# Performance work log

Measured on AMD Instinct MI355X. Metric: run time of the kernel, lower is better.

The kernel has to match this reference:

```python
import jax, jax.numpy as jnp
import numpy as np

B, C, H, W, K = 16, 64, 192, 192, 3

def setup_inputs() -> dict:
    key = jax.random.key(0)
    k1, k2, k3, k4 = jax.random.split(key, 4)
    x = jax.random.normal(k1, (B, C, H, W), dtype=jnp.float32)
    DoT = jax.random.uniform(k2, (B,), dtype=jnp.float32)
    W0 = jax.random.normal(k3, (C, C, K, K), dtype=jnp.float32) * 0.05
    W1 = jax.random.normal(k4, (C, C, K, K), dtype=jnp.float32) * 0.05
    return {"x": x, "DoT": DoT, "W0": W0, "W1": W1}

def reference(x, DoT, W0, W1):
    # Per-sample blended kernels: [B, C_o, C_i, K, K]
    d = DoT[:, None, None, None, None]
    kernel = (1.0 - d) * W0[None] + d * W1[None]

    def conv_one(xi, ki):
        # xi: [C_i, H, W], ki: [C_o, C_i, K, K]
        out = jax.lax.conv_general_dilated(
            xi[None], ki,
            window_strides=(1, 1),
            padding=((1, 1), (1, 1)),
            dimension_numbers=("NCHW", "OIHW", "NCHW"),
        )
        return out[0]

    y = jax.vmap(conv_one)(x, kernel)  # [B, C_o, H, W]
    return y
```

## Files before the change

kernel.cpp:

```cpp
#include <hip/hip_runtime.h>
#include <hip/hip_bf16.h>
#include <stdint.h>

#define NB 16
#define NC 64
#define NH 192
#define NW 192
#define NKDIM 576

typedef __bf16 bf16x8 __attribute__((ext_vector_type(8)));
typedef __bf16 bf16x4 __attribute__((ext_vector_type(4)));
typedef float  f32x4  __attribute__((ext_vector_type(4)));

static __device__ __forceinline__ __bf16 f2bf(float f) { return (__bf16)f; }

__global__ __launch_bounds__(256)
void blend_kernel(const float* __restrict__ W0, const float* __restrict__ W1,
                  const float* __restrict__ DoT, __bf16* __restrict__ A) {
    int idx = blockIdx.x * 256 + threadIdx.x;
    int k   = idx % NKDIM;
    int co  = (idx / NKDIM) % NC;
    int b   = idx / (NKDIM * NC);
    int tap = k >> 6;
    int ci  = k & 63;
    float d  = DoT[b];
    int wi   = (co * NC + ci) * 9 + tap;
    float v  = (1.0f - d) * W0[wi] + d * W1[wi];
    A[idx] = f2bf(v);
}

__global__ __launch_bounds__(256)
void nhwc_cvt_kernel(const float* __restrict__ x, __bf16* __restrict__ xt) {
    __shared__ float tile[64 * 68];

    const int b  = blockIdx.z;
    const int h  = blockIdx.y;
    const int wt = blockIdx.x * 64;
    const int t  = threadIdx.x;

    {
        const int ci = t & 63;
        const int wq = t >> 6;
        const float* src = x + ((size_t)(b * NC + ci) * NH + h) * NW + wt;
        #pragma unroll
        for (int w4l = 0; w4l < 4; ++w4l) {
            const int w4 = wq * 4 + w4l;
            f32x4 v = *(const f32x4*)(src + w4 * 4);
            #pragma unroll
            for (int j = 0; j < 4; ++j)
                tile[(w4 * 4 + j) * 68 + ci] = v[j];
        }
    }
    __syncthreads();

    __bf16* dst = xt + ((size_t)(b * NH + h) * NW + wt) * NC;
    #pragma unroll
    for (int it = 0; it < 2; ++it) {
        const int c   = it * 256 + t;
        const int w   = c >> 3;
        const int cig = c & 7;
        f32x4 v0 = *(const f32x4*)&tile[w * 68 + cig * 8];
        f32x4 v1 = *(const f32x4*)&tile[w * 68 + cig * 8 + 4];
        bf16x8 pk = { f2bf(v0[0]), f2bf(v0[1]), f2bf(v0[2]), f2bf(v0[3]),
                      f2bf(v1[0]), f2bf(v1[1]), f2bf(v1[2]), f2bf(v1[3]) };
        *(bf16x8*)(dst + (size_t)w * NC + cig * 8) = pk;
    }
}

__global__ __launch_bounds__(512, 4)
void conv_nhwc_kernel(const __bf16* __restrict__ xt, const __bf16* __restrict__ A,
                      float* __restrict__ out) {
    __shared__ __bf16 xs[4 * 66 * 8 * 8];

    const int b  = blockIdx.z;
    const int h0 = blockIdx.y * 2;
    const int w0 = blockIdx.x * 64;

    const int tid  = threadIdx.x;
    const int lane = tid & 63;
    const int wave = tid >> 6;

    {
        #pragma unroll
        for (int it = 0; it < 4; ++it) {
            const int c   = it * 512 + tid;
            const int r   = c / 528;
            const int rem = c - r * 528;
            const int w   = rem >> 3;
            const int g   = rem & 7;
            const int gr  = h0 - 1 + r;
            const int gw  = w0 - 1 + w;
            const bool ok = (gr >= 0) && (gr < NH) && (gw >= 0) && (gw < NW);
            bf16x8 v = {};
            if (ok)
                v = *(const bf16x8*)(xt + ((size_t)(b * NH + gr) * NW + gw) * NC + g * 8);
            *(bf16x8*)&xs[(((r * 66 + w) * 8) + (g ^ (w & 7))) * 8] = v;
        }
        if (tid < 64) {
            const int c   = 2048 + tid;
            const int r   = 3;
            const int rem = c - 3 * 528;
            const int w   = rem >> 3;
            const int g   = rem & 7;
            const int gr  = h0 + 2;
            const int gw  = w0 - 1 + w;
            const bool ok = (gr < NH) && (gw < NW);
            bf16x8 v = {};
            if (ok)
                v = *(const bf16x8*)(xt + ((size_t)(b * NH + gr) * NW + gw) * NC + g * 8);
            *(bf16x8*)&xs[(((r * 66 + w) * 8) + (g ^ (w & 7))) * 8] = v;
        }
    }

    const int mt   = wave & 3;
    const int nh   = wave >> 2;
    const int n    = lane & 15;
    const int quad = lane >> 4;

    const __bf16* Ap = A + ((size_t)b * NC + mt * 16 + n) * NKDIM + quad * 8;
    bf16x8 afr[9][2];
    #pragma unroll
    for (int tap = 0; tap < 9; ++tap)
        #pragma unroll
        for (int ch = 0; ch < 2; ++ch)
            afr[tap][ch] = *(const bf16x8*)(Ap + tap * 64 + ch * 32);

    __syncthreads();

    f32x4 acc[4];
    #pragma unroll
    for (int nt = 0; nt < 4; ++nt) acc[nt] = (f32x4){0.f, 0.f, 0.f, 0.f};

    #pragma unroll
    for (int tap = 0; tap < 9; ++tap) {
        const int dh  = tap / 3;
        const int dw  = tap - dh * 3;
        const int row = nh + dh;
        #pragma unroll
        for (int ch = 0; ch < 2; ++ch) {
            #pragma unroll
            for (int nt = 0; nt < 4; ++nt) {
                const int wl = dw + nt * 16 + n;
                const int gp = (ch * 4 + quad) ^ (wl & 7);
                bf16x8 bfr = *(const bf16x8*)&xs[(((row * 66 + wl) * 8) + gp) * 8];
                acc[nt] = __builtin_amdgcn_mfma_f32_16x16x32_bf16(
                    afr[tap][ch], bfr, acc[nt], 0, 0, 0);
            }
        }
    }

    const int h = h0 + nh;
    float* ob = out + (size_t)b * NC * NH * NW + (size_t)h * NW + w0;
    #pragma unroll
    for (int reg = 0; reg < 4; ++reg) {
        const int co = mt * 16 + quad * 4 + reg;
        float* orow = ob + (size_t)co * NH * NW;
        #pragma unroll
        for (int nt = 0; nt < 4; ++nt) {
            orow[nt * 16 + n] = acc[nt][reg];
        }
    }
}

__global__ __launch_bounds__(512, 4)
void conv_nchw_kernel(const float* __restrict__ x, const __bf16* __restrict__ A,
                      float* __restrict__ out) {
    __shared__ __bf16 xs[4 * 66 * 72];

    const int b  = blockIdx.z;
    const int h0 = blockIdx.y * 2;
    const int w0 = blockIdx.x * 64;

    const int tid  = threadIdx.x;
    const int lane = tid & 63;
    const int wave = tid >> 6;

    {
        const int r  = tid >> 7;
        const int s  = tid & 127;
        const int gr = h0 - 1 + r;
        const bool rowok = (gr >= 0) && (gr < NH);
        const float* xb = x + (size_t)b * NC * NH * NW + (ptrdiff_t)gr * NW;

        #pragma unroll
        for (int j = 0; j < 8; ++j) {
            const int p   = j * 128 + s;
            const int wl  = p & 63;
            const int ci4 = p >> 6;
            const int gw  = w0 - 1 + wl;
            const bool ok = rowok && (gw >= 0);
            float v0 = ok ? xb[(size_t)(ci4 * 4 + 0) * NH * NW + gw] : 0.0f;
            float v1 = ok ? xb[(size_t)(ci4 * 4 + 1) * NH * NW + gw] : 0.0f;
            float v2 = ok ? xb[(size_t)(ci4 * 4 + 2) * NH * NW + gw] : 0.0f;
            float v3 = ok ? xb[(size_t)(ci4 * 4 + 3) * NH * NW + gw] : 0.0f;
            bf16x4 pk = { f2bf(v0), f2bf(v1), f2bf(v2), f2bf(v3) };
            const int g  = ci4 >> 1;
            const int gp = g ^ ((wl >> 3) & 7);
            *(bf16x4*)&xs[(r * 66 + wl) * 72 + gp * 8 + (ci4 & 1) * 4] = pk;
        }
        if (s < 32) {
            const int wl  = 64 + (s & 1);
            const int ci4 = s >> 1;
            const int gw  = w0 - 1 + wl;
            const bool ok = rowok && (gw < NW);
            float v0 = ok ? xb[(size_t)(ci4 * 4 + 0) * NH * NW + gw] : 0.0f;
            float v1 = ok ? xb[(size_t)(ci4 * 4 + 1) * NH * NW + gw] : 0.0f;
            float v2 = ok ? xb[(size_t)(ci4 * 4 + 2) * NH * NW + gw] : 0.0f;
            float v3 = ok ? xb[(size_t)(ci4 * 4 + 3) * NH * NW + gw] : 0.0f;
            bf16x4 pk = { f2bf(v0), f2bf(v1), f2bf(v2), f2bf(v3) };
            const int g  = ci4 >> 1;
            const int gp = g ^ ((wl >> 3) & 7);
            *(bf16x4*)&xs[(r * 66 + wl) * 72 + gp * 8 + (ci4 & 1) * 4] = pk;
        }
    }

    const int mt   = wave & 3;
    const int nh   = wave >> 2;
    const int n    = lane & 15;
    const int quad = lane >> 4;

    const __bf16* Ap = A + ((size_t)b * NC + mt * 16 + n) * NKDIM + quad * 8;
    bf16x8 afr[9][2];
    #pragma unroll
    for (int tap = 0; tap < 9; ++tap)
        #pragma unroll
        for (int ch = 0; ch < 2; ++ch)
            afr[tap][ch] = *(const bf16x8*)(Ap + tap * 64 + ch * 32);

    __syncthreads();

    f32x4 acc[4];
    #pragma unroll
    for (int nt = 0; nt < 4; ++nt) acc[nt] = (f32x4){0.f, 0.f, 0.f, 0.f};

    #pragma unroll
    for (int tap = 0; tap < 9; ++tap) {
        const int dh  = tap / 3;
        const int dw  = tap - dh * 3;
        const int row = nh + dh;
        #pragma unroll
        for (int ch = 0; ch < 2; ++ch) {
            const int g = ch * 4 + quad;
            #pragma unroll
            for (int nt = 0; nt < 4; ++nt) {
                const int wl = dw + nt * 16 + n;
                const int gp = g ^ ((wl >> 3) & 7);
                bf16x8 bfr = *(const bf16x8*)&xs[(row * 66 + wl) * 72 + gp * 8];
                acc[nt] = __builtin_amdgcn_mfma_f32_16x16x32_bf16(
                    afr[tap][ch], bfr, acc[nt], 0, 0, 0);
            }
        }
    }

    const int h = h0 + nh;
    float* ob = out + (size_t)b * NC * NH * NW + (size_t)h * NW + w0;
    #pragma unroll
    for (int reg = 0; reg < 4; ++reg) {
        const int co = mt * 16 + quad * 4 + reg;
        float* orow = ob + (size_t)co * NH * NW;
        #pragma unroll
        for (int nt = 0; nt < 4; ++nt) {
            orow[nt * 16 + n] = acc[nt][reg];
        }
    }
}

extern "C" void kernel_launch(void* const* d_in, const int* in_sizes, int n_in,
                              void* d_out, int out_size, void* d_ws, size_t ws_size,
                              hipStream_t stream) {
    const float* x   = (const float*)d_in[0];
    const float* DoT = (const float*)d_in[1];
    const float* W0  = (const float*)d_in[2];
    const float* W1  = (const float*)d_in[3];
    float* out = (float*)d_out;

    const size_t A_BYTES  = (size_t)NB * NC * NKDIM * 2;
    const size_t XT_BYTES = (size_t)NB * NH * NW * NC * 2;
    __bf16* A  = (__bf16*)d_ws;
    __bf16* xt = (__bf16*)((char*)d_ws + A_BYTES);

    blend_kernel<<<dim3((NB * NC * NKDIM) / 256), 256, 0, stream>>>(W0, W1, DoT, A);

    if (ws_size >= A_BYTES + XT_BYTES) {
        nhwc_cvt_kernel<<<dim3(NW / 64, NH, NB), dim3(256), 0, stream>>>(x, xt);
        conv_nhwc_kernel<<<dim3(NW / 64, NH / 2, NB), dim3(512), 0, stream>>>(xt, A, out);
    } else {
        conv_nchw_kernel<<<dim3(NW / 64, NH / 2, NB), dim3(512), 0, stream>>>(x, A, out);
    }
}
```

Baseline: 373.5 us.

## Fuse NHWC conversion into conv, tile four rows per block with swizzled grid

Drops the separate NCHW-to-NHWC bf16 conversion pass. The conv kernel now reads fp32 NCHW input directly, converting it to bf16 in shared memory, and each block covers four output rows instead of two, so each wave computes two rows. This reduces halo re-reads and removes a full intermediate write and read. It also streams per-tap weight fragments from global memory with one-tap prefetch instead of holding all 18 in registers, and swizzles a 1D grid so neighbouring blocks land on different XCDs. The trade-offs are a larger shared tile (about 57 KB), which may limit occupancy, and strided per-channel global loads.

```diff
diff --git a/kernel.cpp b/kernel.cpp
--- a/kernel.cpp
+++ b/kernel.cpp
@@ -29,184 +29,59 @@
     A[idx] = f2bf(v);
 }
 
-__global__ __launch_bounds__(256)
-void nhwc_cvt_kernel(const float* __restrict__ x, __bf16* __restrict__ xt) {
-    __shared__ float tile[64 * 68];
+__global__ __launch_bounds__(512, 4)
+void conv_fused_kernel(const float* __restrict__ x, const __bf16* __restrict__ A,
+                       float* __restrict__ out) {
+    __shared__ __align__(16) __bf16 xs[6 * 66 * 72];
 
-    const int b  = blockIdx.z;
-    const int h  = blockIdx.y;
-    const int wt = blockIdx.x * 64;
-    const int t  = threadIdx.x;
+    const int lid = blockIdx.x;
+    const int swz = (lid & 7) * 288 + (lid >> 3);
+    const int b   = swz / 144;
+    const int rem = swz - b * 144;
+    const int by  = rem / 3;
+    const int bx  = rem - by * 3;
 
-    {
-        const int ci = t & 63;
-        const int wq = t >> 6;
-        const float* src = x + ((size_t)(b * NC + ci) * NH + h) * NW + wt;
-        #pragma unroll
-        for (int w4l = 0; w4l < 4; ++w4l) {
-            const int w4 = wq * 4 + w4l;
-            f32x4 v = *(const f32x4*)(src + w4 * 4);
-            #pragma unroll
-            for (int j = 0; j < 4; ++j)
-                tile[(w4 * 4 + j) * 68 + ci] = v[j];
-        }
-    }
-    __syncthreads();
-
-    __bf16* dst = xt + ((size_t)(b * NH + h) * NW + wt) * NC;
-    #pragma unroll
-    for (int it = 0; it < 2; ++it) {
-        const int c   = it * 256 + t;
-        const int w   = c >> 3;
-        const int cig = c & 7;
-        f32x4 v0 = *(const f32x4*)&tile[w * 68 + cig * 8];
-        f32x4 v1 = *(const f32x4*)&tile[w * 68 + cig * 8 + 4];
-        bf16x8 pk = { f2bf(v0[0]), f2bf(v0[1]), f2bf(v0[2]), f2bf(v0[3]),
-                      f2bf(v1[0]), f2bf(v1[1]), f2bf(v1[2]), f2bf(v1[3]) };
-        *(bf16x8*)(dst + (size_t)w * NC + cig * 8) = pk;
-    }
-}
-
-__global__ __launch_bounds__(512, 4)
-void conv_nhwc_kernel(const __bf16* __restrict__ xt, const __bf16* __restrict__ A,
-                      float* __restrict__ out) {
-    __shared__ __bf16 xs[4 * 66 * 8 * 8];
-
-    const int b  = blockIdx.z;
-    const int h0 = blockIdx.y * 2;
-    const int w0 = blockIdx.x * 64;
+    const int h0 = by * 4;
+    const int w0 = bx * 64;
 
     const int tid  = threadIdx.x;
     const int lane = tid & 63;
     const int wave = tid >> 6;
 
     {
+        const float* xb0 = x + (size_t)b * NC * NH * NW;
         #pragma unroll
-        for (int it = 0; it < 4; ++it) {
-            const int c   = it * 512 + tid;
-            const int r   = c / 528;
-            const int rem = c - r * 528;
-            const int w   = rem >> 3;
-            const int g   = rem & 7;
+        for (int it = 0; it < 12; ++it) {
+            const int q   = it * 512 + tid;
+            const int r   = q >> 10;
+            const int rm  = q & 1023;
+            const int wl  = rm & 63;
+            const int ci4 = rm >> 6;
             const int gr  = h0 - 1 + r;
-            const int gw  = w0 - 1 + w;
-            const bool ok = (gr >= 0) && (gr < NH) && (gw >= 0) && (gw < NW);
-            bf16x8 v = {};
-            if (ok)
-                v = *(const bf16x8*)(xt + ((size_t)(b * NH + gr) * NW + gw) * NC + g * 8);
-            *(bf16x8*)&xs[(((r * 66 + w) * 8) + (g ^ (w & 7))) * 8] = v;
-        }
-        if (tid < 64) {
-            const int c   = 2048 + tid;
-            const int r   = 3;
-            const int rem = c - 3 * 528;
-            const int w   = rem >> 3;
-            const int g   = rem & 7;
-            const int gr  = h0 + 2;
-            const int gw  = w0 - 1 + w;
-            const bool ok = (gr < NH) && (gw < NW);
-            bf16x8 v = {};
-            if (ok)
-                v = *(const bf16x8*)(xt + ((size_t)(b * NH + gr) * NW + gw) * NC + g * 8);
-            *(bf16x8*)&xs[(((r * 66 + w) * 8) + (g ^ (w & 7))) * 8] = v;
-        }
-    }
-
-    const int mt   = wave & 3;
-    const int nh   = wave >> 2;
-    const int n    = lane & 15;
-    const int quad = lane >> 4;
-
-    const __bf16* Ap = A + ((size_t)b * NC + mt * 16 + n) * NKDIM + quad * 8;
-    bf16x8 afr[9][2];
-    #pragma unroll
-    for (int tap = 0; tap < 9; ++tap)
-        #pragma unroll
-        for (int ch = 0; ch < 2; ++ch)
-            afr[tap][ch] = *(const bf16x8*)(Ap + tap * 64 + ch * 32);
-
-    __syncthreads();
-
-    f32x4 acc[4];
-    #pragma unroll
-    for (int nt = 0; nt < 4; ++nt) acc[nt] = (f32x4){0.f, 0.f, 0.f, 0.f};
-
-    #pragma unroll
-    for (int tap = 0; tap < 9; ++tap) {
-        const int dh  = tap / 3;
-        const int dw  = tap - dh * 3;
-        const int row = nh + dh;
-        #pragma unroll
-        for (int ch = 0; ch < 2; ++ch) {
-            #pragma unroll
-            for (int nt = 0; nt < 4; ++nt) {
-                const int wl = dw + nt * 16 + n;
-                const int gp = (ch * 4 + quad) ^ (wl & 7);
-                bf16x8 bfr = *(const bf16x8*)&xs[(((row * 66 + wl) * 8) + gp) * 8];
-                acc[nt] = __builtin_amdgcn_mfma_f32_16x16x32_bf16(
-                    afr[tap][ch], bfr, acc[nt], 0, 0, 0);
-            }
-        }
-    }
-
-    const int h = h0 + nh;
-    float* ob = out + (size_t)b * NC * NH * NW + (size_t)h * NW + w0;
-    #pragma unroll
-    for (int reg = 0; reg < 4; ++reg) {
-        const int co = mt * 16 + quad * 4 + reg;
-        float* orow = ob + (size_t)co * NH * NW;
-        #pragma unroll
-        for (int nt = 0; nt < 4; ++nt) {
-            orow[nt * 16 + n] = acc[nt][reg];
-        }
-    }
-}
-
-__global__ __launch_bounds__(512, 4)
-void conv_nchw_kernel(const float* __restrict__ x, const __bf16* __restrict__ A,
-                      float* __restrict__ out) {
-    __shared__ __bf16 xs[4 * 66 * 72];
-
-    const int b  = blockIdx.z;
-    const int h0 = blockIdx.y * 2;
-    const int w0 = blockIdx.x * 64;
-
-    const int tid  = threadIdx.x;
-    const int lane = tid & 63;
-    const int wave = tid >> 6;
-
-    {
-        const int r  = tid >> 7;
-        const int s  = tid & 127;
-        const int gr = h0 - 1 + r;
-        const bool rowok = (gr >= 0) && (gr < NH);
-        const float* xb = x + (size_t)b * NC * NH * NW + (ptrdiff_t)gr * NW;
-
-        #pragma unroll
-        for (int j = 0; j < 8; ++j) {
-            const int p   = j * 128 + s;
-            const int wl  = p & 63;
-            const int ci4 = p >> 6;
             const int gw  = w0 - 1 + wl;
-            const bool ok = rowok && (gw >= 0);
-            float v0 = ok ? xb[(size_t)(ci4 * 4 + 0) * NH * NW + gw] : 0.0f;
-            float v1 = ok ? xb[(size_t)(ci4 * 4 + 1) * NH * NW + gw] : 0.0f;
-            float v2 = ok ? xb[(size_t)(ci4 * 4 + 2) * NH * NW + gw] : 0.0f;
-            float v3 = ok ? xb[(size_t)(ci4 * 4 + 3) * NH * NW + gw] : 0.0f;
+            const bool ok = (gr >= 0) && (gr < NH) && (gw >= 0);
+            const float* xp = xb0 + ((size_t)(ci4 * 4) * NH + gr) * NW + gw;
+            float v0 = ok ? xp[0] : 0.0f;
+            float v1 = ok ? xp[(size_t)NH * NW] : 0.0f;
+            float v2 = ok ? xp[2 * (size_t)NH * NW] : 0.0f;
+            float v3 = ok ? xp[3 * (size_t)NH * NW] : 0.0f;
             bf16x4 pk = { f2bf(v0), f2bf(v1), f2bf(v2), f2bf(v3) };
             const int g  = ci4 >> 1;
             const int gp = g ^ ((wl >> 3) & 7);
             *(bf16x4*)&xs[(r * 66 + wl) * 72 + gp * 8 + (ci4 & 1) * 4] = pk;
         }
-        if (s < 32) {
-            const int wl  = 64 + (s & 1);
-            const int ci4 = s >> 1;
+        if (tid < 192) {
+            const int wl  = 64 + (tid & 1);
+            const int ci4 = (tid >> 1) & 15;
+            const int r   = tid >> 5;
+            const int gr  = h0 - 1 + r;
             const int gw  = w0 - 1 + wl;
-            const bool ok = rowok && (gw < NW);
-            float v0 = ok ? xb[(size_t)(ci4 * 4 + 0) * NH * NW + gw] : 0.0f;
-            float v1 = ok ? xb[(size_t)(ci4 * 4 + 1) * NH * NW + gw] : 0.0f;
-            float v2 = ok ? xb[(size_t)(ci4 * 4 + 2) * NH * NW + gw] : 0.0f;
-            float v3 = ok ? xb[(size_t)(ci4 * 4 + 3) * NH * NW + gw] : 0.0f;
+            const bool ok = (gr >= 0) && (gr < NH) && (gw < NW);
+            const float* xp = xb0 + ((size_t)(ci4 * 4) * NH + gr) * NW + gw;
+            float v0 = ok ? xp[0] : 0.0f;
+            float v1 = ok ? xp[(size_t)NH * NW] : 0.0f;
+            float v2 = ok ? xp[2 * (size_t)NH * NW] : 0.0f;
+            float v3 = ok ? xp[3 * (size_t)NH * NW] : 0.0f;
             bf16x4 pk = { f2bf(v0), f2bf(v1), f2bf(v2), f2bf(v3) };
             const int g  = ci4 >> 1;
             const int gp = g ^ ((wl >> 3) & 7);
@@ -220,47 +95,57 @@
     const int quad = lane >> 4;
 
     const __bf16* Ap = A + ((size_t)b * NC + mt * 16 + n) * NKDIM + quad * 8;
-    bf16x8 afr[9][2];
+    bf16x8 a0 = *(const bf16x8*)(Ap + 0);
+    bf16x8 a1 = *(const bf16x8*)(Ap + 32);
+
+    f32x4 acc[2][4];
     #pragma unroll
-    for (int tap = 0; tap < 9; ++tap)
+    for (int rr = 0; rr < 2; ++rr)
         #pragma unroll
-        for (int ch = 0; ch < 2; ++ch)
-            afr[tap][ch] = *(const bf16x8*)(Ap + tap * 64 + ch * 32);
+        for (int nt = 0; nt < 4; ++nt)
+            acc[rr][nt] = (f32x4){0.f, 0.f, 0.f, 0.f};
 
     __syncthreads();
 
-    f32x4 acc[4];
-    #pragma unroll
-    for (int nt = 0; nt < 4; ++nt) acc[nt] = (f32x4){0.f, 0.f, 0.f, 0.f};
-
     #pragma unroll
     for (int tap = 0; tap < 9; ++tap) {
-        const int dh  = tap / 3;
-        const int dw  = tap - dh * 3;
-        const int row = nh + dh;
+        const int tn = (tap < 8) ? tap + 1 : 8;
+        const bf16x8 na0 = *(const bf16x8*)(Ap + tn * 64);
+        const bf16x8 na1 = *(const bf16x8*)(Ap + tn * 64 + 32);
+
+        const int dh = tap / 3;
+        const int dw = tap - dh * 3;
         #pragma unroll
-        for (int ch = 0; ch < 2; ++ch) {
-            const int g = ch * 4 + quad;
+        for (int rr = 0; rr < 2; ++rr) {
+            const int row = nh * 2 + rr + dh;
             #pragma unroll
             for (int nt = 0; nt < 4; ++nt) {
                 const int wl = dw + nt * 16 + n;
-                const int gp = g ^ ((wl >> 3) & 7);
-                bf16x8 bfr = *(const bf16x8*)&xs[(row * 66 + wl) * 72 + gp * 8];
-                acc[nt] = __builtin_amdgcn_mfma_f32_16x16x32_bf16(
-                    afr[tap][ch], bfr, acc[nt], 0, 0, 0);
+                const int sw = (wl >> 3) & 7;
+                const int base = (row * 66 + wl) * 72;
+                bf16x8 b0 = *(const bf16x8*)&xs[base + ((0 * 4 + quad) ^ sw) * 8];
+                bf16x8 b1 = *(const bf16x8*)&xs[base + ((1 * 4 + quad) ^ sw) * 8];
+                acc[rr][nt] = __builtin_amdgcn_mfma_f32_16x16x32_bf16(
+                    a0, b0, acc[rr][nt], 0, 0, 0);
+                acc[rr][nt] = __builtin_amdgcn_mfma_f32_16x16x32_bf16(
+                    a1, b1, acc[rr][nt], 0, 0, 0);
             }
         }
+        a0 = na0; a1 = na1;
     }
 
-    const int h = h0 + nh;
-    float* ob = out + (size_t)b * NC * NH * NW + (size_t)h * NW + w0;
     #pragma unroll
-    for (int reg = 0; reg < 4; ++reg) {
-        const int co = mt * 16 + quad * 4 + reg;
-        float* orow = ob + (size_t)co * NH * NW;
+    for (int rr = 0; rr < 2; ++rr) {
+        const int h = h0 + nh * 2 + rr;
+        float* ob = out + (size_t)b * NC * NH * NW + (size_t)h * NW + w0;
         #pragma unroll
-        for (int nt = 0; nt < 4; ++nt) {
-            orow[nt * 16 + n] = acc[nt][reg];
+        for (int reg = 0; reg < 4; ++reg) {
+            const int co = mt * 16 + quad * 4 + reg;
+            float* orow = ob + (size_t)co * NH * NW;
+            #pragma unroll
+            for (int nt = 0; nt < 4; ++nt) {
+                orow[nt * 16 + n] = acc[rr][nt][reg];
+            }
         }
     }
 }
@@ -274,17 +159,9 @@
     const float* W1  = (const float*)d_in[3];
     float* out = (float*)d_out;
 
-    const size_t A_BYTES  = (size_t)NB * NC * NKDIM * 2;
-    const size_t XT_BYTES = (size_t)NB * NH * NW * NC * 2;
-    __bf16* A  = (__bf16*)d_ws;
-    __bf16* xt = (__bf16*)((char*)d_ws + A_BYTES);
+    __bf16* A = (__bf16*)d_ws;
 
     blend_kernel<<<dim3((NB * NC * NKDIM) / 256), 256, 0, stream>>>(W0, W1, DoT, A);
 
-    if (ws_size >= A_BYTES + XT_BYTES) {
-        nhwc_cvt_kernel<<<dim3(NW / 64, NH, NB), dim3(256), 0, stream>>>(x, xt);
-        conv_nhwc_kernel<<<dim3(NW / 64, NH / 2, NB), dim3(512), 0, stream>>>(xt, A, out);
-    } else {
-        conv_nchw_kernel<<<dim3(NW / 64, NH / 2, NB), dim3(512), 0, stream>>>(x, A, out);
-    }
+    conv_fused_kernel<<<dim3(2304, 1, 1), dim3(512), 0, stream>>>(x, A, out);
 }
```

Result: slower. 535.7 us (+43.4%).

## Compute four output rows per block and stream A fragments per tap

Applied to the files above, without the earlier changes.

Each block of the NHWC conv kernel now covers 4 output rows instead of 2, with each wave handling 2 rows. This reuses each A (weight) fragment across two rows and cuts halo reloading from 4/2 to 6/4 input rows per output row. A fragments are no longer all held in registers (9x2 vectors); they are prefetched one tap ahead, which lowers register pressure. The grid has half as many blocks, which may reduce occupancy and load balance across CUs.

```diff
diff --git a/kernel.cpp b/kernel.cpp
--- a/kernel.cpp
+++ b/kernel.cpp
@@ -70,10 +70,10 @@
 __global__ __launch_bounds__(512, 4)
 void conv_nhwc_kernel(const __bf16* __restrict__ xt, const __bf16* __restrict__ A,
                       float* __restrict__ out) {
-    __shared__ __bf16 xs[4 * 66 * 8 * 8];
+    __shared__ __align__(16) __bf16 xs[6 * 66 * 8 * 8];
 
     const int b  = blockIdx.z;
-    const int h0 = blockIdx.y * 2;
+    const int h0 = blockIdx.y * 4;
     const int w0 = blockIdx.x * 64;
 
     const int tid  = threadIdx.x;
@@ -82,7 +82,7 @@
 
     {
         #pragma unroll
-        for (int it = 0; it < 4; ++it) {
+        for (int it = 0; it < 6; ++it) {
             const int c   = it * 512 + tid;
             const int r   = c / 528;
             const int rem = c - r * 528;
@@ -96,13 +96,12 @@
                 v = *(const bf16x8*)(xt + ((size_t)(b * NH + gr) * NW + gw) * NC + g * 8);
             *(bf16x8*)&xs[(((r * 66 + w) * 8) + (g ^ (w & 7))) * 8] = v;
         }
-        if (tid < 64) {
-            const int c   = 2048 + tid;
-            const int r   = 3;
-            const int rem = c - 3 * 528;
+        if (tid < 96) {
+            const int r   = 5;
+            const int rem = 432 + tid;
             const int w   = rem >> 3;
             const int g   = rem & 7;
-            const int gr  = h0 + 2;
+            const int gr  = h0 + 4;
             const int gw  = w0 - 1 + w;
             const bool ok = (gr < NH) && (gw < NW);
             bf16x8 v = {};
@@ -118,46 +117,57 @@
     const int quad = lane >> 4;
 
     const __bf16* Ap = A + ((size_t)b * NC + mt * 16 + n) * NKDIM + quad * 8;
-    bf16x8 afr[9][2];
-    #pragma unroll
-    for (int tap = 0; tap < 9; ++tap)
-        #pragma unroll
-        for (int ch = 0; ch < 2; ++ch)
-            afr[tap][ch] = *(const bf16x8*)(Ap + tap * 64 + ch * 32);
+    bf16x8 a0 = *(const bf16x8*)(Ap + 0);
+    bf16x8 a1 = *(const bf16x8*)(Ap + 32);
+
+    f32x4 acc[2][4];
+    #pragma unroll
+    for (int rr = 0; rr < 2; ++rr)
+        #pragma unroll
+        for (int nt = 0; nt < 4; ++nt)
+            acc[rr][nt] = (f32x4){0.f, 0.f, 0.f, 0.f};
 
     __syncthreads();
 
-    f32x4 acc[4];
-    #pragma unroll
-    for (int nt = 0; nt < 4; ++nt) acc[nt] = (f32x4){0.f, 0.f, 0.f, 0.f};
-
     #pragma unroll
     for (int tap = 0; tap < 9; ++tap) {
-        const int dh  = tap / 3;
-        const int dw  = tap - dh * 3;
-        const int row = nh + dh;
-        #pragma unroll
-        for (int ch = 0; ch < 2; ++ch) {
+        const int tn = (tap < 8) ? tap + 1 : 8;
+        const bf16x8 na0 = *(const bf16x8*)(Ap + tn * 64);
+        const bf16x8 na1 = *(const bf16x8*)(Ap + tn * 64 + 32);
+
+        const int dh = tap / 3;
+        const int dw = tap - dh * 3;
+        #pragma unroll
+        for (int rr = 0; rr < 2; ++rr) {
+            const int row = nh * 2 + rr + dh;
             #pragma unroll
             for (int nt = 0; nt < 4; ++nt) {
                 const int wl = dw + nt * 16 + n;
-                const int gp = (ch * 4 + quad) ^ (wl & 7);
-                bf16x8 bfr = *(const bf16x8*)&xs[(((row * 66 + wl) * 8) + gp) * 8];
-                acc[nt] = __builtin_amdgcn_mfma_f32_16x16x32_bf16(
-                    afr[tap][ch], bfr, acc[nt], 0, 0, 0);
+                const int sw = wl & 7;
+                const int base = ((row * 66 + wl) * 8) * 8;
+                bf16x8 b0 = *(const bf16x8*)&xs[base + ((0 * 4 + quad) ^ sw) * 8];
+                acc[rr][nt] = __builtin_amdgcn_mfma_f32_16x16x32_bf16(
+                    a0, b0, acc[rr][nt], 0, 0, 0);
+                bf16x8 b1 = *(const bf16x8*)&xs[base + ((1 * 4 + quad) ^ sw) * 8];
+                acc[rr][nt] = __builtin_amdgcn_mfma_f32_16x16x32_bf16(
+                    a1, b1, acc[rr][nt], 0, 0, 0);
             }
         }
-    }
-
-    const int h = h0 + nh;
-    float* ob = out + (size_t)b * NC * NH * NW + (size_t)h * NW + w0;
-    #pragma unroll
-    for (int reg = 0; reg < 4; ++reg) {
-        const int co = mt * 16 + quad * 4 + reg;
-        float* orow = ob + (size_t)co * NH * NW;
-        #pragma unroll
-        for (int nt = 0; nt < 4; ++nt) {
-            orow[nt * 16 + n] = acc[nt][reg];
+        a0 = na0; a1 = na1;
+    }
+
+    #pragma unroll
+    for (int rr = 0; rr < 2; ++rr) {
+        const int h = h0 + nh * 2 + rr;
+        float* ob = out + (size_t)b * NC * NH * NW + (size_t)h * NW + w0;
+        #pragma unroll
+        for (int reg = 0; reg < 4; ++reg) {
+            const int co = mt * 16 + quad * 4 + reg;
+            float* orow = ob + (size_t)co * NH * NW;
+            #pragma unroll
+            for (int nt = 0; nt < 4; ++nt) {
+                orow[nt * 16 + n] = acc[rr][nt][reg];
+            }
         }
     }
 }
@@ -283,7 +293,7 @@
 
     if (ws_size >= A_BYTES + XT_BYTES) {
         nhwc_cvt_kernel<<<dim3(NW / 64, NH, NB), dim3(256), 0, stream>>>(x, xt);
-        conv_nhwc_kernel<<<dim3(NW / 64, NH / 2, NB), dim3(512), 0, stream>>>(xt, A, out);
+        conv_nhwc_kernel<<<dim3(NW / 64, NH / 4, NB), dim3(512), 0, stream>>>(xt, A, out);
     } else {
         conv_nchw_kernel<<<dim3(NW / 64, NH / 2, NB), dim3(512), 0, stream>>>(x, A, out);
     }
```

Measured after the change: 444.3 us. +18.9%, slower.

## Slide conv blocks down 12-row strips with a ring-buffered halo and prefetch

Applied to the files above, without the earlier changes.

Each NHWC conv block now covers a 12-row strip instead of 2 rows. It keeps a 6-row ring buffer in shared memory and reuses the overlapping halo rows between steps. The next two input rows are loaded into registers while the current step's MFMAs run, and the per-sample weight fragments are loaded once per strip instead of once per two rows. The grid is six times smaller, which lowers parallelism (768 blocks), and each step now needs two barriers.

```diff
diff --git a/kernel.cpp b/kernel.cpp
--- a/kernel.cpp
+++ b/kernel.cpp
@@ -7,6 +7,9 @@
 #define NH 192
 #define NW 192
 #define NKDIM 576
+
+#define STRIP 12
+#define NSTEP 6
 
 typedef __bf16 bf16x8 __attribute__((ext_vector_type(8)));
 typedef __bf16 bf16x4 __attribute__((ext_vector_type(4)));
@@ -68,55 +71,51 @@
 }
 
 __global__ __launch_bounds__(512, 4)
-void conv_nhwc_kernel(const __bf16* __restrict__ xt, const __bf16* __restrict__ A,
-                      float* __restrict__ out) {
-    __shared__ __bf16 xs[4 * 66 * 8 * 8];
+void conv_slide_kernel(const __bf16* __restrict__ xt, const __bf16* __restrict__ A,
+                       float* __restrict__ out) {
+    __shared__ __align__(16) __bf16 xs[6 * 66 * 64];
 
     const int b  = blockIdx.z;
-    const int h0 = blockIdx.y * 2;
+    const int h0 = blockIdx.y * STRIP;
     const int w0 = blockIdx.x * 64;
 
     const int tid  = threadIdx.x;
     const int lane = tid & 63;
     const int wave = tid >> 6;
-
-    {
-        #pragma unroll
-        for (int it = 0; it < 4; ++it) {
-            const int c   = it * 512 + tid;
-            const int r   = c / 528;
-            const int rem = c - r * 528;
-            const int w   = rem >> 3;
-            const int g   = rem & 7;
-            const int gr  = h0 - 1 + r;
-            const int gw  = w0 - 1 + w;
-            const bool ok = (gr >= 0) && (gr < NH) && (gw >= 0) && (gw < NW);
-            bf16x8 v = {};
-            if (ok)
-                v = *(const bf16x8*)(xt + ((size_t)(b * NH + gr) * NW + gw) * NC + g * 8);
-            *(bf16x8*)&xs[(((r * 66 + w) * 8) + (g ^ (w & 7))) * 8] = v;
-        }
-        if (tid < 64) {
-            const int c   = 2048 + tid;
-            const int r   = 3;
-            const int rem = c - 3 * 528;
-            const int w   = rem >> 3;
-            const int g   = rem & 7;
-            const int gr  = h0 + 2;
-            const int gw  = w0 - 1 + w;
-            const bool ok = (gr < NH) && (gw < NW);
-            bf16x8 v = {};
-            if (ok)
-                v = *(const bf16x8*)(xt + ((size_t)(b * NH + gr) * NW + gw) * NC + g * 8);
-            *(bf16x8*)&xs[(((r * 66 + w) * 8) + (g ^ (w & 7))) * 8] = v;
-        }
-    }
-
     const int mt   = wave & 3;
     const int nh   = wave >> 2;
     const int n    = lane & 15;
     const int quad = lane >> 4;
 
+    const __bf16* xb = xt + (size_t)b * NH * NW * NC;
+
+    const int sw_  = tid >> 3;
+    const int sg_  = tid & 7;
+    const int tlr_ = tid >> 4;
+    const int tw_  = 64 + ((tid >> 3) & 1);
+
+    #define LDCHUNK(j, w, g, v)                                                 \
+        {   const int gr_ = h0 - 1 + (j);                                       \
+            const int gw_ = w0 - 1 + (w);                                       \
+            v = (bf16x8){};                                                     \
+            if (gr_ >= 0 && gr_ < NH && gw_ >= 0 && gw_ < NW)                   \
+                v = *(const bf16x8*)(xb + ((size_t)gr_ * NW + gw_) * NC + (g) * 8); }
+    #define STCHUNK(slot, w, g, v)                                              \
+        *(bf16x8*)&xs[((((slot) * 66 + (w)) * 8) + ((g) ^ ((w) & 7))) * 8] = (v);
+
+    {
+        #pragma unroll
+        for (int it = 0; it < 3; ++it) {
+            bf16x8 v; LDCHUNK(it, sw_, sg_, v);
+            STCHUNK(it, sw_, sg_, v);
+        }
+        if (tid < 48) {
+            const int j = tid >> 4;
+            bf16x8 v; LDCHUNK(j, tw_, sg_, v);
+            STCHUNK(j, tw_, sg_, v);
+        }
+    }
+
     const __bf16* Ap = A + ((size_t)b * NC + mt * 16 + n) * NKDIM + quad * 8;
     bf16x8 afr[9][2];
     #pragma unroll
@@ -125,41 +124,66 @@
         for (int ch = 0; ch < 2; ++ch)
             afr[tap][ch] = *(const bf16x8*)(Ap + tap * 64 + ch * 32);
 
-    __syncthreads();
-
-    f32x4 acc[4];
-    #pragma unroll
-    for (int nt = 0; nt < 4; ++nt) acc[nt] = (f32x4){0.f, 0.f, 0.f, 0.f};
-
-    #pragma unroll
-    for (int tap = 0; tap < 9; ++tap) {
-        const int dh  = tap / 3;
-        const int dw  = tap - dh * 3;
-        const int row = nh + dh;
-        #pragma unroll
-        for (int ch = 0; ch < 2; ++ch) {
+    bf16x8 r0_, r1_, rt_ = {};
+    LDCHUNK(3, sw_, sg_, r0_);
+    LDCHUNK(4, sw_, sg_, r1_);
+    if (tid < 32) { LDCHUNK(3 + tlr_, tw_, sg_, rt_); }
+
+    float* const ob0 = out + (size_t)b * NC * NH * NW + w0;
+
+    #pragma unroll
+    for (int s = 0; s < NSTEP; ++s) {
+        STCHUNK((2 * s + 3) % 6, sw_, sg_, r0_);
+        STCHUNK((2 * s + 4) % 6, sw_, sg_, r1_);
+        if (tid < 32) { STCHUNK((2 * s + 3 + tlr_) % 6, tw_, sg_, rt_); }
+        __syncthreads();
+
+        if (s < NSTEP - 1) {
+            LDCHUNK(2 * s + 5, sw_, sg_, r0_);
+            LDCHUNK(2 * s + 6, sw_, sg_, r1_);
+            if (tid < 32) { LDCHUNK(2 * s + 5 + tlr_, tw_, sg_, rt_); }
+        }
+
+        f32x4 acc[4];
+        #pragma unroll
+        for (int nt = 0; nt < 4; ++nt) acc[nt] = (f32x4){0.f, 0.f, 0.f, 0.f};
+
+        #pragma unroll
+        for (int tap = 0; tap < 9; ++tap) {
+            const int dh   = tap / 3;
+            const int dw   = tap - dh * 3;
+            const int slot = (2 * s + nh + dh) % 6;
             #pragma unroll
             for (int nt = 0; nt < 4; ++nt) {
-                const int wl = dw + nt * 16 + n;
-                const int gp = (ch * 4 + quad) ^ (wl & 7);
-                bf16x8 bfr = *(const bf16x8*)&xs[(((row * 66 + wl) * 8) + gp) * 8];
+                const int wl   = dw + nt * 16 + n;
+                const int sw   = wl & 7;
+                const int base = ((slot * 66 + wl) * 8) * 8;
+                bf16x8 b0 = *(const bf16x8*)&xs[base + ((0 * 4 + quad) ^ sw) * 8];
                 acc[nt] = __builtin_amdgcn_mfma_f32_16x16x32_bf16(
-                    afr[tap][ch], bfr, acc[nt], 0, 0, 0);
+                    afr[tap][0], b0, acc[nt], 0, 0, 0);
+                bf16x8 b1 = *(const bf16x8*)&xs[base + ((1 * 4 + quad) ^ sw) * 8];
+                acc[nt] = __builtin_amdgcn_mfma_f32_16x16x32_bf16(
+                    afr[tap][1], b1, acc[nt], 0, 0, 0);
             }
         }
-    }
-
-    const int h = h0 + nh;
-    float* ob = out + (size_t)b * NC * NH * NW + (size_t)h * NW + w0;
-    #pragma unroll
-    for (int reg = 0; reg < 4; ++reg) {
-        const int co = mt * 16 + quad * 4 + reg;
-        float* orow = ob + (size_t)co * NH * NW;
-        #pragma unroll
-        for (int nt = 0; nt < 4; ++nt) {
-            orow[nt * 16 + n] = acc[nt][reg];
-        }
-    }
+
+        {
+            const int y = h0 + 2 * s + nh;
+            float* ob = ob0 + (size_t)y * NW;
+            #pragma unroll
+            for (int reg = 0; reg < 4; ++reg) {
+                const int co = mt * 16 + quad * 4 + reg;
+                float* orow = ob + (size_t)co * NH * NW;
+                #pragma unroll
+                for (int nt = 0; nt < 4; ++nt) {
+                    orow[nt * 16 + n] = acc[nt][reg];
+                }
+            }
+        }
+        __syncthreads();
+    }
+    #undef LDCHUNK
+    #undef STCHUNK
 }
 
 __global__ __launch_bounds__(512, 4)
@@ -283,7 +307,7 @@
 
     if (ws_size >= A_BYTES + XT_BYTES) {
         nhwc_cvt_kernel<<<dim3(NW / 64, NH, NB), dim3(256), 0, stream>>>(x, xt);
-        conv_nhwc_kernel<<<dim3(NW / 64, NH / 2, NB), dim3(512), 0, stream>>>(xt, A, out);
+        conv_slide_kernel<<<dim3(NW / 64, NH / STRIP, NB), dim3(512), 0, stream>>>(xt, A, out);
     } else {
         conv_nchw_kernel<<<dim3(NW / 64, NH / 2, NB), dim3(512), 0, stream>>>(x, A, out);
     }
```

Result: slower. 454.6 us (+21.7%).
